# Kernel optimization log

Measured on AMD Instinct MI355X. Metric: run time of the kernel, lower is better.

## Reference

```python
import jax, jax.numpy as jnp
import numpy as np
import math

B, N, C = 32, 576, 1024
INNER, H = 256, 4
HD = INNER // H
ALPHA = 5.0
EPS = 1e-5

def _layer_norm(x, w, b):
    mu = jnp.mean(x, axis=-1, keepdims=True)
    var = jnp.mean((x - mu) ** 2, axis=-1, keepdims=True)
    return (x - mu) * jax.lax.rsqrt(var + EPS) * w + b

def setup_inputs() -> dict:
    key = jax.random.key(0)
    ks = jax.random.split(key, 20)
    def lin(k, out_d, in_d):
        scale = math.sqrt(6.0 / (in_d + out_d))
        return jax.random.uniform(k, (out_d, in_d), jnp.float32, -scale, scale)
    return {
        'query_features': jax.random.normal(ks[0], (B, N, C), jnp.float32),
        'support_features': jax.random.normal(ks[1], (B, N, C), jnp.float32),
        'support_mask_weights': jax.random.uniform(ks[2], (B, N), jnp.float32),
        'ln_q_w': jnp.ones((C,), jnp.float32), 'ln_q_b': jnp.zeros((C,), jnp.float32),
        'ln_s_w': jnp.ones((C,), jnp.float32), 'ln_s_b': jnp.zeros((C,), jnp.float32),
        'Wq': lin(ks[3], INNER, C), 'bq': jnp.zeros((INNER,), jnp.float32),
        'Wk': lin(ks[4], INNER, C), 'bk': jnp.zeros((INNER,), jnp.float32),
        'Wv': lin(ks[5], INNER, C), 'bv': jnp.zeros((INNER,), jnp.float32),
        'Wo': lin(ks[6], C, INNER), 'bo': jnp.zeros((C,), jnp.float32),
        'Wg': 0.02 * jax.random.normal(ks[7], (C, C), jnp.float32),
        'bg': jnp.full((C,), -1.0, jnp.float32),
    }

def reference(query_features, support_features, support_mask_weights,
              ln_q_w, ln_q_b, ln_s_w, ln_s_b,
              Wq, bq, Wk, bk, Wv, bv, Wo, bo, Wg, bg):
    q = _layer_norm(query_features, ln_q_w, ln_q_b)
    s = _layer_norm(support_features, ln_s_w, ln_s_b)
    Q = (q @ Wq.T + bq).reshape(B, N, H, HD).transpose(0, 2, 1, 3)  # (B,H,N,HD)
    K = (s @ Wk.T + bk).reshape(B, N, H, HD).transpose(0, 2, 1, 3)
    V = (s @ Wv.T + bv).reshape(B, N, H, HD).transpose(0, 2, 1, 3)
    logits = jnp.einsum('bhnd,bhmd->bhnm', Q, K) / math.sqrt(HD)
    logits = logits + ALPHA * support_mask_weights[:, None, None, :]
    attn = jax.nn.softmax(logits, axis=-1)
    ctx = jnp.einsum('bhnm,bhmd->bhnd', attn, V).transpose(0, 2, 1, 3).reshape(B, N, INNER)
    out = ctx @ Wo.T + bo
    gate = jax.nn.sigmoid(query_features @ Wg.T + bg)
    enhanced = query_features + gate * out
    return enhanced, attn
```

## Files before the change

kernel.cpp:

```cpp
#include <hip/hip_runtime.h>
#include <hip/hip_bf16.h>
#include <math.h>

#define B_ 32
#define N_ 576
#define C_ 1024
#define INNER_ 256
#define H_ 4
#define HD_ 64
#define M_ (B_*N_)
#define ALPHA_ 5.0f
#define EPS_ 1e-5f

typedef __attribute__((ext_vector_type(8))) short bf16x8;
typedef __attribute__((ext_vector_type(4))) float f32x4;
typedef __attribute__((ext_vector_type(4))) unsigned int u32x4;
typedef unsigned short u16;

__device__ inline u16 bfbits(float x) {
    union { __hip_bfloat16 h; u16 u; } c; c.h = __float2bfloat16(x); return c.u;
}
__device__ inline unsigned pack2bf(float a, float b) {
    return (unsigned)bfbits(a) | ((unsigned)bfbits(b) << 16);
}

template<int WRITE_RAW>
__global__ void ln_fused_kernel(const float* __restrict__ X, const float* __restrict__ w,
                                const float* __restrict__ b, u16* __restrict__ outln,
                                u16* __restrict__ outraw) {
    int row = blockIdx.x * 4 + (threadIdx.x >> 6);
    int lane = threadIdx.x & 63;
    const float* xp = X + (size_t)row * C_;
    float4 v[4];
    #pragma unroll
    for (int j = 0; j < 4; ++j) v[j] = *(const float4*)(xp + lane*4 + j*256);
    float s = 0.f, s2 = 0.f;
    #pragma unroll
    for (int j = 0; j < 4; ++j) {
        s  += v[j].x + v[j].y + v[j].z + v[j].w;
        s2 += v[j].x*v[j].x + v[j].y*v[j].y + v[j].z*v[j].z + v[j].w*v[j].w;
    }
    #pragma unroll
    for (int m = 32; m; m >>= 1) {
        s  += __shfl_xor(s,  m, 64);
        s2 += __shfl_xor(s2, m, 64);
    }
    float mean = s * (1.f/C_);
    float rs = rsqrtf(s2 * (1.f/C_) - mean*mean + EPS_);
    #pragma unroll
    for (int j = 0; j < 4; ++j) {
        int k = lane*4 + j*256;
        float4 wv = *(const float4*)(w + k);
        float4 bv = *(const float4*)(b + k);
        ushort4 o;
        o.x = bfbits((v[j].x - mean)*rs*wv.x + bv.x);
        o.y = bfbits((v[j].y - mean)*rs*wv.y + bv.y);
        o.z = bfbits((v[j].z - mean)*rs*wv.z + bv.z);
        o.w = bfbits((v[j].w - mean)*rs*wv.w + bv.w);
        *(ushort4*)(outln + (size_t)row*C_ + k) = o;
        if (WRITE_RAW) {
            ushort4 r4;
            r4.x = bfbits(v[j].x); r4.y = bfbits(v[j].y);
            r4.z = bfbits(v[j].z); r4.w = bfbits(v[j].w);
            *(ushort4*)(outraw + (size_t)row*C_ + k) = r4;
        }
    }
}

__global__ void cvt_weights_kernel(const float* __restrict__ Wq, const float* __restrict__ Wk,
                                   const float* __restrict__ Wv, const float* __restrict__ Wo,
                                   const float* __restrict__ Wg,
                                   const float* __restrict__ bk, const float* __restrict__ bv,
                                   u16* __restrict__ Wq_b, u16* __restrict__ Wkv_b,
                                   u16* __restrict__ Wo_b, u16* __restrict__ Wg_b,
                                   float* __restrict__ bkv) {
    if (blockIdx.x == 0 && threadIdx.x < 128) {
        float4 t = (threadIdx.x < 64) ? ((const float4*)bk)[threadIdx.x]
                                      : ((const float4*)bv)[threadIdx.x - 64];
        ((float4*)bkv)[threadIdx.x] = t;
    }
    int g = blockIdx.x * 256 + threadIdx.x;
    const float* src; u16* dst; size_t off;
    if (g < 32768)       { src = Wq; dst = Wq_b;          off = (size_t)g*8; }
    else if (g < 65536)  { src = Wk; dst = Wkv_b;         off = (size_t)(g-32768)*8; }
    else if (g < 98304)  { src = Wv; dst = Wkv_b + 262144; off = (size_t)(g-65536)*8; }
    else if (g < 131072) { src = Wo; dst = Wo_b;          off = (size_t)(g-98304)*8; }
    else                 { src = Wg; dst = Wg_b;          off = (size_t)(g-131072)*8; }
    float4 a0 = *(const float4*)(src + off);
    float4 a1 = *(const float4*)(src + off + 4);
    union { u16 s[8]; u32x4 v; } o;
    o.s[0] = bfbits(a0.x); o.s[1] = bfbits(a0.y); o.s[2] = bfbits(a0.z); o.s[3] = bfbits(a0.w);
    o.s[4] = bfbits(a1.x); o.s[5] = bfbits(a1.y); o.s[6] = bfbits(a1.z); o.s[7] = bfbits(a1.w);
    *(u32x4*)(dst + off) = o.v;
}

template<int KDIM, bool F32A>
__device__ inline void gemm_accum(const void* __restrict__ Ap, const u16* __restrict__ Bw,
                                  int row0, int col0, int tid, int lane, int wm, int wn,
                                  u16 (&Asm)[128][72], u16 (&Bsm)[128][72],
                                  f32x4 (&acc)[4][4]) {
    for (int k0 = 0; k0 < KDIM; k0 += 64) {
        #pragma unroll
        for (int i = 0; i < 4; ++i) {
            int s = tid + i*256;
            int r = s >> 3, cg = (s & 7) * 8;
            u32x4 vb = *(const u32x4*)(Bw + (size_t)(col0 + r)*KDIM + k0 + cg);
            if (F32A) {
                const float* a = (const float*)Ap + (size_t)(row0 + r)*KDIM + k0 + cg;
                float4 a0 = *(const float4*)a;
                float4 a1 = *(const float4*)(a + 4);
                union { u16 s[8]; u32x4 v; } o;
                o.s[0]=bfbits(a0.x); o.s[1]=bfbits(a0.y); o.s[2]=bfbits(a0.z); o.s[3]=bfbits(a0.w);
                o.s[4]=bfbits(a1.x); o.s[5]=bfbits(a1.y); o.s[6]=bfbits(a1.z); o.s[7]=bfbits(a1.w);
                *(u32x4*)&Asm[r][cg] = o.v;
            } else {
                *(u32x4*)&Asm[r][cg] =
                    *(const u32x4*)((const u16*)Ap + (size_t)(row0 + r)*KDIM + k0 + cg);
            }
            *(u32x4*)&Bsm[r][cg] = vb;
        }
        __syncthreads();
        #pragma unroll
        for (int ks = 0; ks < 64; ks += 32) {
            bf16x8 af[4], bfr[4];
            #pragma unroll
            for (int i = 0; i < 4; ++i)
                af[i] = *(const bf16x8*)&Asm[wm + i*16 + (lane & 15)][ks + (lane >> 4)*8];
            #pragma unroll
            for (int j = 0; j < 4; ++j)
                bfr[j] = *(const bf16x8*)&Bsm[wn + j*16 + (lane & 15)][ks + (lane >> 4)*8];
            #pragma unroll
            for (int i = 0; i < 4; ++i)
                #pragma unroll
                for (int j = 0; j < 4; ++j)
                    acc[i][j] = __builtin_amdgcn_mfma_f32_16x16x32_bf16(
                        af[i], bfr[j], acc[i][j], 0, 0, 0);
        }
        __syncthreads();
    }
}

template<int NOUT, int KDIM>
__global__ __launch_bounds__(256, 2)
void mfma_gemm_kernel(const u16* __restrict__ A, const u16* __restrict__ Bw,
                      const float* __restrict__ bias, u16* __restrict__ Out) {
    __shared__ u16 Asm[128][72];
    __shared__ u16 Bsm[128][72];
    int tid = threadIdx.x;
    int lane = tid & 63, wid = tid >> 6;
    int wm = (wid >> 1) * 64, wn = (wid & 1) * 64;
    int row0 = blockIdx.y * 128, col0 = blockIdx.x * 128;
    f32x4 acc[4][4] = {};
    gemm_accum<KDIM, false>(A, Bw, row0, col0, tid, lane, wm, wn, Asm, Bsm, acc);
    #pragma unroll
    for (int i = 0; i < 4; ++i) {
        #pragma unroll
        for (int j = 0; j < 4; ++j) {
            int col = col0 + wn + j*16 + (lane & 15);
            float bb = bias[col];
            #pragma unroll
            for (int r = 0; r < 4; ++r) {
                int row = row0 + wm + i*16 + (lane >> 4)*4 + r;
                Out[(size_t)row * NOUT + col] = bfbits(acc[i][j][r] + bb);
            }
        }
    }
}

__global__ __launch_bounds__(256, 2)
void final_fused_kernel(const float* __restrict__ query, const u16* __restrict__ Wg_b,
                        const float* __restrict__ bg,
                        const u16* __restrict__ ctxb, const u16* __restrict__ Wo_b,
                        const float* __restrict__ bo, float* __restrict__ out) {
    __shared__ u16 Asm[128][72];
    __shared__ u16 Bsm[128][72];
    int tid = threadIdx.x;
    int lane = tid & 63, wid = tid >> 6;
    int wm = (wid >> 1) * 64, wn = (wid & 1) * 64;
    int row0 = blockIdx.y * 128, col0 = blockIdx.x * 128;
    f32x4 acc_o[4][4] = {};
    f32x4 acc_g[4][4] = {};
    gemm_accum<INNER_, false>(ctxb, Wo_b, row0, col0, tid, lane, wm, wn, Asm, Bsm, acc_o);
    gemm_accum<C_, true>(query, Wg_b, row0, col0, tid, lane, wm, wn, Asm, Bsm, acc_g);
    #pragma unroll
    for (int i = 0; i < 4; ++i) {
        #pragma unroll
        for (int j = 0; j < 4; ++j) {
            int col = col0 + wn + j*16 + (lane & 15);
            float bgv = bg[col], bov = bo[col];
            #pragma unroll
            for (int r = 0; r < 4; ++r) {
                int row = row0 + wm + i*16 + (lane >> 4)*4 + r;
                size_t idx = (size_t)row * C_ + col;
                float g = 1.f / (1.f + expf(-(acc_g[i][j][r] + bgv)));
                out[idx] = query[idx] + g * (acc_o[i][j][r] + bov);
            }
        }
    }
}

__device__ inline void stage_v_half(const u16* __restrict__ KV, u16* __restrict__ Vt,
                                    int b, int h, int HF, int tid) {
    #pragma unroll
    for (int i = 0; i < 9; ++i) {
        int c = tid + i*256;
        int k = c >> 3;
        int d0 = (c & 7) * 8;
        union { u32x4 v; u16 s[8]; } u;
        u.v = *(const u32x4*)(KV + ((size_t)(b*N_ + HF*288 + k))*512 + 256 + h*HD_ + d0);
        #pragma unroll
        for (int e = 0; e < 8; ++e)
            Vt[(d0 + e)*296 + k] = u.s[e];
    }
}

template<int HF>
__device__ inline void pv_half(const unsigned (&pk)[36][2], f32x4 (&cacc)[4],
                               const u16* __restrict__ Vt, int lane) {
    int s1 = (lane & 15) + ((lane & 16) << 1);
    int s2 = s1 + 16;
    bool hi = (lane & 32) != 0;
    #pragma unroll
    for (int t9 = 0; t9 < 9; ++t9) {
        const int t = HF*9 + t9;
        unsigned A01 = __shfl((int)pk[2*t  ][0], s1, 64);
        unsigned A23 = __shfl((int)pk[2*t  ][1], s1, 64);
        unsigned B01 = __shfl((int)pk[2*t+1][0], s1, 64);
        unsigned B23 = __shfl((int)pk[2*t+1][1], s1, 64);
        unsigned C01 = __shfl((int)pk[2*t  ][0], s2, 64);
        unsigned C23 = __shfl((int)pk[2*t  ][1], s2, 64);
        unsigned D01 = __shfl((int)pk[2*t+1][0], s2, 64);
        unsigned D23 = __shfl((int)pk[2*t+1][1], s2, 64);
        union { unsigned w[4]; bf16x8 v; } bu;
        bu.w[0] = hi ? B01 : A01;
        bu.w[1] = hi ? B23 : A23;
        bu.w[2] = hi ? D01 : C01;
        bu.w[3] = hi ? D23 : C23;
        int colb = 32*t - 288*HF + 8*(lane >> 4);
        #pragma unroll
        for (int dt = 0; dt < 4; ++dt) {
            bf16x8 a = *(const bf16x8*)&Vt[(16*dt + (lane & 15))*296 + colb];
            cacc[dt] = __builtin_amdgcn_mfma_f32_16x16x32_bf16(a, bu.v, cacc[dt], 0, 0, 0);
        }
    }
}

__global__ __launch_bounds__(256, 2)
void attn_mfma_kernel(const u16* __restrict__ Qbf, const u16* __restrict__ KV,
                      const float* __restrict__ mask,
                      float* __restrict__ attn_out, u16* __restrict__ ctxb) {
    __shared__ u16 Vt[64*296];
    __shared__ float Msk[576];
    int tid = threadIdx.x;
    int lane = tid & 63, wid = tid >> 6;
    int bh = blockIdx.y, b = bh >> 2, h = bh & 3;
    int q0 = blockIdx.x * 64;
    int g = lane >> 4;
    int qrow = q0 + wid*16 + (lane & 15);

    if (tid < 144) {
        float4 mv = *(const float4*)(mask + b*N_ + tid*4);
        *(float4*)&Msk[tid*4] = make_float4(ALPHA_*mv.x, ALPHA_*mv.y, ALPHA_*mv.z, ALPHA_*mv.w);
    }
    stage_v_half(KV, Vt, b, h, 0, tid);
    __syncthreads();

    const u16* qp = Qbf + ((size_t)(b*N_) + qrow)*INNER_ + h*HD_ + g*8;
    bf16x8 qf0 = *(const bf16x8*)qp;
    bf16x8 qf1 = *(const bf16x8*)(qp + 32);

    f32x4 acc[36];
    #pragma unroll
    for (int T = 0; T < 36; ++T) acc[T] = (f32x4){0.f, 0.f, 0.f, 0.f};

    const u16* kp = KV + ((size_t)(b*N_) + (lane & 15))*512 + h*HD_ + g*8;
    bf16x8 kb[2][2];
    kb[0][0] = *(const bf16x8*)(kp);
    kb[0][1] = *(const bf16x8*)(kp + 32);
    kb[1][0] = *(const bf16x8*)(kp + 16*512);
    kb[1][1] = *(const bf16x8*)(kp + 16*512 + 32);
    #pragma unroll
    for (int T = 0; T < 36; ++T) {
        bf16x8 n0, n1;
        if (T + 2 < 36) {
            n0 = *(const bf16x8*)(kp + (size_t)(T+2)*16*512);
            n1 = *(const bf16x8*)(kp + (size_t)(T+2)*16*512 + 32);
        }
        acc[T] = __builtin_amdgcn_mfma_f32_16x16x32_bf16(kb[T&1][0], qf0, acc[T], 0, 0, 0);
        acc[T] = __builtin_amdgcn_mfma_f32_16x16x32_bf16(kb[T&1][1], qf1, acc[T], 0, 0, 0);
        if (T + 2 < 36) { kb[T&1][0] = n0; kb[T&1][1] = n1; }
    }

    float m = -1e30f;
    #pragma unroll
    for (int T = 0; T < 36; ++T) {
        float4 mk = *(const float4*)&Msk[16*T + 4*g];
        acc[T][0] = acc[T][0]*0.125f + mk.x;
        acc[T][1] = acc[T][1]*0.125f + mk.y;
        acc[T][2] = acc[T][2]*0.125f + mk.z;
        acc[T][3] = acc[T][3]*0.125f + mk.w;
        m = fmaxf(m, fmaxf(fmaxf(acc[T][0], acc[T][1]), fmaxf(acc[T][2], acc[T][3])));
    }
    m = fmaxf(m, __shfl_xor(m, 16, 64));
    m = fmaxf(m, __shfl_xor(m, 32, 64));

    float l = 0.f;
    #pragma unroll
    for (int T = 0; T < 36; ++T) {
        acc[T][0] = expf(acc[T][0] - m);
        acc[T][1] = expf(acc[T][1] - m);
        acc[T][2] = expf(acc[T][2] - m);
        acc[T][3] = expf(acc[T][3] - m);
        l += acc[T][0] + acc[T][1] + acc[T][2] + acc[T][3];
    }
    l += __shfl_xor(l, 16, 64);
    l += __shfl_xor(l, 32, 64);
    float inv = 1.f / l;

    unsigned pk[36][2];
    float* ap = attn_out + ((size_t)bh*N_ + qrow)*N_;
    #pragma unroll
    for (int T = 0; T < 36; ++T) {
        float e0 = acc[T][0]*inv, e1 = acc[T][1]*inv;
        float e2 = acc[T][2]*inv, e3 = acc[T][3]*inv;
        *(float4*)(ap + 16*T + 4*g) = make_float4(e0, e1, e2, e3);
        pk[T][0] = pack2bf(e0, e1);
        pk[T][1] = pack2bf(e2, e3);
    }

    f32x4 cacc[4] = {};
    pv_half<0>(pk, cacc, Vt, lane);
    __syncthreads();
    stage_v_half(KV, Vt, b, h, 1, tid);
    __syncthreads();
    pv_half<1>(pk, cacc, Vt, lane);

    u16* cp = ctxb + ((size_t)(b*N_) + qrow)*INNER_ + h*HD_ + 4*g;
    #pragma unroll
    for (int dt = 0; dt < 4; ++dt) {
        ushort4 o;
        o.x = bfbits(cacc[dt][0]);
        o.y = bfbits(cacc[dt][1]);
        o.z = bfbits(cacc[dt][2]);
        o.w = bfbits(cacc[dt][3]);
        *(ushort4*)(cp + 16*dt) = o;
    }
}

extern "C" void kernel_launch(void* const* d_in, const int* in_sizes, int n_in,
                              void* d_out, int out_size, void* d_ws, size_t ws_size,
                              hipStream_t stream) {
    const float* query   = (const float*)d_in[0];
    const float* support = (const float*)d_in[1];
    const float* mask    = (const float*)d_in[2];
    const float* ln_q_w  = (const float*)d_in[3];
    const float* ln_q_b  = (const float*)d_in[4];
    const float* ln_s_w  = (const float*)d_in[5];
    const float* ln_s_b  = (const float*)d_in[6];
    const float* Wq      = (const float*)d_in[7];
    const float* bq      = (const float*)d_in[8];
    const float* Wk      = (const float*)d_in[9];
    const float* bk      = (const float*)d_in[10];
    const float* Wv      = (const float*)d_in[11];
    const float* bv      = (const float*)d_in[12];
    const float* Wo      = (const float*)d_in[13];
    const float* bo      = (const float*)d_in[14];
    const float* Wg      = (const float*)d_in[15];
    const float* bg      = (const float*)d_in[16];

    float* out      = (float*)d_out;
    float* attn_out = out + (size_t)M_ * C_;

    char* w = (char*)d_ws;
    u16* Aq    = (u16*)w;  w += (size_t)M_*C_*2;
    u16* As_   = (u16*)w;  w += (size_t)M_*C_*2;
    u16* Wq_b  = (u16*)w;  w += (size_t)INNER_*C_*2;
    u16* Wkv_b = (u16*)w;  w += (size_t)2*INNER_*C_*2;
    u16* Wo_b  = (u16*)w;  w += (size_t)C_*INNER_*2;
    u16* Wg_b  = (u16*)w;  w += (size_t)C_*C_*2;
    float* bkv = (float*)w; w += 512*4;
    u16* Qbf   = (u16*)w;  w += (size_t)M_*INNER_*2;
    u16* KVbf  = (u16*)w;  w += (size_t)M_*2*INNER_*2;
    u16* ctxb  = (u16*)w;  w += (size_t)M_*INNER_*2;

    ln_fused_kernel<0><<<dim3(M_/4), dim3(256), 0, stream>>>(query,   ln_q_w, ln_q_b, Aq,  nullptr);
    ln_fused_kernel<0><<<dim3(M_/4), dim3(256), 0, stream>>>(support, ln_s_w, ln_s_b, As_, nullptr);

    cvt_weights_kernel<<<dim3(1024), dim3(256), 0, stream>>>(
        Wq, Wk, Wv, Wo, Wg, bk, bv, Wq_b, Wkv_b, Wo_b, Wg_b, bkv);

    mfma_gemm_kernel<INNER_, C_><<<dim3(INNER_/128, M_/128), dim3(256), 0, stream>>>(
        Aq, Wq_b, bq, Qbf);
    mfma_gemm_kernel<2*INNER_, C_><<<dim3(2*INNER_/128, M_/128), dim3(256), 0, stream>>>(
        As_, Wkv_b, bkv, KVbf);

    attn_mfma_kernel<<<dim3(N_/64, B_*H_), dim3(256), 0, stream>>>(
        Qbf, KVbf, mask, attn_out, ctxb);

    final_fused_kernel<<<dim3(C_/128, M_/128), dim3(256), 0, stream>>>(
        query, Wg_b, bg, ctxb, Wo_b, bo, out);
}
```

Before: 368.4 us.

## Remap GEMM and attention blocks per XCD and pre-convert query to bf16 in LN

Adds an XCD-aware block index remap so consecutive row tiles run on the same XCD, aiming at better L2 reuse of shared A/B tiles across the GEMMs and the attention kernel. The query LayerNorm kernel now also writes a raw bf16 copy of the query. The final gate GEMM reads that bf16 copy instead of loading fp32 and converting on every tile. The cost is an extra M×C bf16 write in the LN pass and more workspace memory.

```diff
diff --git a/kernel.cpp b/kernel.cpp
--- a/kernel.cpp
+++ b/kernel.cpp
@@ -22,6 +22,15 @@
 }
 __device__ inline unsigned pack2bf(float a, float b) {
     return (unsigned)bfbits(a) | ((unsigned)bfbits(b) << 16);
+}
+
+template<int GX, int GY>
+__device__ inline void xcd_remap(int& col, int& row) {
+    int f = blockIdx.y * GX + blockIdx.x;
+    int xcd = f & 7;
+    int slot = f >> 3;
+    col = slot % GX;
+    row = xcd * (GY >> 3) + slot / GX;
 }
 
 template<int WRITE_RAW>
@@ -94,8 +103,8 @@
     *(u32x4*)(dst + off) = o.v;
 }
 
-template<int KDIM, bool F32A>
-__device__ inline void gemm_accum(const void* __restrict__ Ap, const u16* __restrict__ Bw,
+template<int KDIM>
+__device__ inline void gemm_accum(const u16* __restrict__ Ap, const u16* __restrict__ Bw,
                                   int row0, int col0, int tid, int lane, int wm, int wn,
                                   u16 (&Asm)[128][72], u16 (&Bsm)[128][72],
                                   f32x4 (&acc)[4][4]) {
@@ -104,20 +113,8 @@
         for (int i = 0; i < 4; ++i) {
             int s = tid + i*256;
             int r = s >> 3, cg = (s & 7) * 8;
-            u32x4 vb = *(const u32x4*)(Bw + (size_t)(col0 + r)*KDIM + k0 + cg);
-            if (F32A) {
-                const float* a = (const float*)Ap + (size_t)(row0 + r)*KDIM + k0 + cg;
-                float4 a0 = *(const float4*)a;
-                float4 a1 = *(const float4*)(a + 4);
-                union { u16 s[8]; u32x4 v; } o;
-                o.s[0]=bfbits(a0.x); o.s[1]=bfbits(a0.y); o.s[2]=bfbits(a0.z); o.s[3]=bfbits(a0.w);
-                o.s[4]=bfbits(a1.x); o.s[5]=bfbits(a1.y); o.s[6]=bfbits(a1.z); o.s[7]=bfbits(a1.w);
-                *(u32x4*)&Asm[r][cg] = o.v;
-            } else {
-                *(u32x4*)&Asm[r][cg] =
-                    *(const u32x4*)((const u16*)Ap + (size_t)(row0 + r)*KDIM + k0 + cg);
-            }
-            *(u32x4*)&Bsm[r][cg] = vb;
+            *(u32x4*)&Asm[r][cg] = *(const u32x4*)(Ap + (size_t)(row0 + r)*KDIM + k0 + cg);
+            *(u32x4*)&Bsm[r][cg] = *(const u32x4*)(Bw + (size_t)(col0 + r)*KDIM + k0 + cg);
         }
         __syncthreads();
         #pragma unroll
@@ -140,7 +137,7 @@
     }
 }
 
-template<int NOUT, int KDIM>
+template<int NOUT, int KDIM, int GX, int GY>
 __global__ __launch_bounds__(256, 2)
 void mfma_gemm_kernel(const u16* __restrict__ A, const u16* __restrict__ Bw,
                       const float* __restrict__ bias, u16* __restrict__ Out) {
@@ -149,9 +146,11 @@
     int tid = threadIdx.x;
     int lane = tid & 63, wid = tid >> 6;
     int wm = (wid >> 1) * 64, wn = (wid & 1) * 64;
-    int row0 = blockIdx.y * 128, col0 = blockIdx.x * 128;
+    int bc, br;
+    xcd_remap<GX, GY>(bc, br);
+    int row0 = br * 128, col0 = bc * 128;
     f32x4 acc[4][4] = {};
-    gemm_accum<KDIM, false>(A, Bw, row0, col0, tid, lane, wm, wn, Asm, Bsm, acc);
+    gemm_accum<KDIM>(A, Bw, row0, col0, tid, lane, wm, wn, Asm, Bsm, acc);
     #pragma unroll
     for (int i = 0; i < 4; ++i) {
         #pragma unroll
@@ -168,8 +167,8 @@
 }
 
 __global__ __launch_bounds__(256, 2)
-void final_fused_kernel(const float* __restrict__ query, const u16* __restrict__ Wg_b,
-                        const float* __restrict__ bg,
+void final_fused_kernel(const float* __restrict__ query, const u16* __restrict__ Xq,
+                        const u16* __restrict__ Wg_b, const float* __restrict__ bg,
                         const u16* __restrict__ ctxb, const u16* __restrict__ Wo_b,
                         const float* __restrict__ bo, float* __restrict__ out) {
     __shared__ u16 Asm[128][72];
@@ -177,11 +176,13 @@
     int tid = threadIdx.x;
     int lane = tid & 63, wid = tid >> 6;
     int wm = (wid >> 1) * 64, wn = (wid & 1) * 64;
-    int row0 = blockIdx.y * 128, col0 = blockIdx.x * 128;
+    int bc, br;
+    xcd_remap<8, 144>(bc, br);
+    int row0 = br * 128, col0 = bc * 128;
     f32x4 acc_o[4][4] = {};
     f32x4 acc_g[4][4] = {};
-    gemm_accum<INNER_, false>(ctxb, Wo_b, row0, col0, tid, lane, wm, wn, Asm, Bsm, acc_o);
-    gemm_accum<C_, true>(query, Wg_b, row0, col0, tid, lane, wm, wn, Asm, Bsm, acc_g);
+    gemm_accum<INNER_>(ctxb, Wo_b, row0, col0, tid, lane, wm, wn, Asm, Bsm, acc_o);
+    gemm_accum<C_>(Xq, Wg_b, row0, col0, tid, lane, wm, wn, Asm, Bsm, acc_g);
     #pragma unroll
     for (int i = 0; i < 4; ++i) {
         #pragma unroll
@@ -253,8 +254,10 @@
     __shared__ float Msk[576];
     int tid = threadIdx.x;
     int lane = tid & 63, wid = tid >> 6;
-    int bh = blockIdx.y, b = bh >> 2, h = bh & 3;
-    int q0 = blockIdx.x * 64;
+    int qb, bh;
+    xcd_remap<9, 128>(qb, bh);
+    int b = bh >> 2, h = bh & 3;
+    int q0 = qb * 64;
     int g = lane >> 4;
     int qrow = q0 + wid*16 + (lane & 15);
 
@@ -374,6 +377,7 @@
     char* w = (char*)d_ws;
     u16* Aq    = (u16*)w;  w += (size_t)M_*C_*2;
     u16* As_   = (u16*)w;  w += (size_t)M_*C_*2;
+    u16* Xq    = (u16*)w;  w += (size_t)M_*C_*2;
     u16* Wq_b  = (u16*)w;  w += (size_t)INNER_*C_*2;
     u16* Wkv_b = (u16*)w;  w += (size_t)2*INNER_*C_*2;
     u16* Wo_b  = (u16*)w;  w += (size_t)C_*INNER_*2;
@@ -383,20 +387,20 @@
     u16* KVbf  = (u16*)w;  w += (size_t)M_*2*INNER_*2;
     u16* ctxb  = (u16*)w;  w += (size_t)M_*INNER_*2;
 
-    ln_fused_kernel<0><<<dim3(M_/4), dim3(256), 0, stream>>>(query,   ln_q_w, ln_q_b, Aq,  nullptr);
+    ln_fused_kernel<1><<<dim3(M_/4), dim3(256), 0, stream>>>(query,   ln_q_w, ln_q_b, Aq,  Xq);
     ln_fused_kernel<0><<<dim3(M_/4), dim3(256), 0, stream>>>(support, ln_s_w, ln_s_b, As_, nullptr);
 
     cvt_weights_kernel<<<dim3(1024), dim3(256), 0, stream>>>(
         Wq, Wk, Wv, Wo, Wg, bk, bv, Wq_b, Wkv_b, Wo_b, Wg_b, bkv);
 
-    mfma_gemm_kernel<INNER_, C_><<<dim3(INNER_/128, M_/128), dim3(256), 0, stream>>>(
+    mfma_gemm_kernel<INNER_, C_, 2, 144><<<dim3(2, 144), dim3(256), 0, stream>>>(
         Aq, Wq_b, bq, Qbf);
-    mfma_gemm_kernel<2*INNER_, C_><<<dim3(2*INNER_/128, M_/128), dim3(256), 0, stream>>>(
+    mfma_gemm_kernel<2*INNER_, C_, 4, 144><<<dim3(4, 144), dim3(256), 0, stream>>>(
         As_, Wkv_b, bkv, KVbf);
 
     attn_mfma_kernel<<<dim3(N_/64, B_*H_), dim3(256), 0, stream>>>(
         Qbf, KVbf, mask, attn_out, ctxb);
 
-    final_fused_kernel<<<dim3(C_/128, M_/128), dim3(256), 0, stream>>>(
-        query, Wg_b, bg, ctxb, Wo_b, bo, out);
-}
+    final_fused_kernel<<<dim3(8, 144), dim3(256), 0, stream>>>(
+        query, Xq, Wg_b, bg, ctxb, Wo_b, bo, out);
+}
```

New measurement: 350.9 us. 4.7% less time.

## Merge launches, remap blocks per XCD, use nontemporal stores for outputs

Applied to the files above, without the earlier changes.

Merges the two layer-norm launches into one grid and the Q and KV projection GEMMs into a single launch, which cuts launch overhead and tail effects. Adds an XCD-aware block remap to the GEMM, attention and final kernels so blocks sharing rows of A or the same batch/head land on the same XCD and reuse its L2. Writes the large attention-probability and final outputs with nontemporal stores to avoid polluting cache. The remap assumes the grid splits evenly into 8 XCD groups and that the hardware dispatches blocks round-robin across XCDs.

```diff
diff --git a/kernel.cpp b/kernel.cpp
--- a/kernel.cpp
+++ b/kernel.cpp
@@ -24,10 +24,22 @@
     return (unsigned)bfbits(a) | ((unsigned)bfbits(b) << 16);
 }
 
-template<int WRITE_RAW>
-__global__ void ln_fused_kernel(const float* __restrict__ X, const float* __restrict__ w,
-                                const float* __restrict__ b, u16* __restrict__ outln,
-                                u16* __restrict__ outraw) {
+template<int GX, int GY>
+__device__ inline void xcd_remap(int& col, int& row) {
+    int f = blockIdx.y * GX + blockIdx.x;
+    int xcd = f & 7;
+    int slot = f >> 3;
+    col = slot % GX;
+    row = xcd * (GY >> 3) + slot / GX;
+}
+
+__global__ void ln_fused2_kernel(const float* __restrict__ Xq, const float* __restrict__ Xs,
+                                 const float* __restrict__ wq, const float* __restrict__ bq,
+                                 const float* __restrict__ ws, const float* __restrict__ bs,
+                                 u16* __restrict__ outq, u16* __restrict__ outs) {
+    const float* X; const float* w; const float* b; u16* o;
+    if (blockIdx.y == 0) { X = Xq; w = wq; b = bq; o = outq; }
+    else                 { X = Xs; w = ws; b = bs; o = outs; }
     int row = blockIdx.x * 4 + (threadIdx.x >> 6);
     int lane = threadIdx.x & 63;
     const float* xp = X + (size_t)row * C_;
@@ -52,18 +64,12 @@
         int k = lane*4 + j*256;
         float4 wv = *(const float4*)(w + k);
         float4 bv = *(const float4*)(b + k);
-        ushort4 o;
-        o.x = bfbits((v[j].x - mean)*rs*wv.x + bv.x);
-        o.y = bfbits((v[j].y - mean)*rs*wv.y + bv.y);
-        o.z = bfbits((v[j].z - mean)*rs*wv.z + bv.z);
-        o.w = bfbits((v[j].w - mean)*rs*wv.w + bv.w);
-        *(ushort4*)(outln + (size_t)row*C_ + k) = o;
-        if (WRITE_RAW) {
-            ushort4 r4;
-            r4.x = bfbits(v[j].x); r4.y = bfbits(v[j].y);
-            r4.z = bfbits(v[j].z); r4.w = bfbits(v[j].w);
-            *(ushort4*)(outraw + (size_t)row*C_ + k) = r4;
-        }
+        ushort4 ov;
+        ov.x = bfbits((v[j].x - mean)*rs*wv.x + bv.x);
+        ov.y = bfbits((v[j].y - mean)*rs*wv.y + bv.y);
+        ov.z = bfbits((v[j].z - mean)*rs*wv.z + bv.z);
+        ov.w = bfbits((v[j].w - mean)*rs*wv.w + bv.w);
+        *(ushort4*)(o + (size_t)row*C_ + k) = ov;
     }
 }
 
@@ -140,18 +146,28 @@
     }
 }
 
-template<int NOUT, int KDIM>
 __global__ __launch_bounds__(256, 2)
-void mfma_gemm_kernel(const u16* __restrict__ A, const u16* __restrict__ Bw,
-                      const float* __restrict__ bias, u16* __restrict__ Out) {
+void qkv_gemm_kernel(const u16* __restrict__ Aq, const u16* __restrict__ As,
+                     const u16* __restrict__ Wq_b, const u16* __restrict__ Wkv_b,
+                     const float* __restrict__ bq, const float* __restrict__ bkv,
+                     u16* __restrict__ Qbf, u16* __restrict__ KVbf) {
     __shared__ u16 Asm[128][72];
     __shared__ u16 Bsm[128][72];
     int tid = threadIdx.x;
     int lane = tid & 63, wid = tid >> 6;
     int wm = (wid >> 1) * 64, wn = (wid & 1) * 64;
-    int row0 = blockIdx.y * 128, col0 = blockIdx.x * 128;
+    int bc, br;
+    xcd_remap<6, 144>(bc, br);
+    int row0 = br * 128;
+    bool isQ = (bc < 2);
+    int col0 = (isQ ? bc : bc - 2) * 128;
+    const u16* A  = isQ ? Aq   : As;
+    const u16* Bw = isQ ? Wq_b : Wkv_b;
+    const float* bias = isQ ? bq : bkv;
+    u16* Out = isQ ? Qbf : KVbf;
+    const int NOUT = isQ ? INNER_ : 2*INNER_;
     f32x4 acc[4][4] = {};
-    gemm_accum<KDIM, false>(A, Bw, row0, col0, tid, lane, wm, wn, Asm, Bsm, acc);
+    gemm_accum<C_, false>(A, Bw, row0, col0, tid, lane, wm, wn, Asm, Bsm, acc);
     #pragma unroll
     for (int i = 0; i < 4; ++i) {
         #pragma unroll
@@ -168,8 +184,8 @@
 }
 
 __global__ __launch_bounds__(256, 2)
-void final_fused_kernel(const float* __restrict__ query, const u16* __restrict__ Wg_b,
-                        const float* __restrict__ bg,
+void final_fused_kernel(const float* __restrict__ query,
+                        const u16* __restrict__ Wg_b, const float* __restrict__ bg,
                         const u16* __restrict__ ctxb, const u16* __restrict__ Wo_b,
                         const float* __restrict__ bo, float* __restrict__ out) {
     __shared__ u16 Asm[128][72];
@@ -177,7 +193,9 @@
     int tid = threadIdx.x;
     int lane = tid & 63, wid = tid >> 6;
     int wm = (wid >> 1) * 64, wn = (wid & 1) * 64;
-    int row0 = blockIdx.y * 128, col0 = blockIdx.x * 128;
+    int bc, br;
+    xcd_remap<8, 144>(bc, br);
+    int row0 = br * 128, col0 = bc * 128;
     f32x4 acc_o[4][4] = {};
     f32x4 acc_g[4][4] = {};
     gemm_accum<INNER_, false>(ctxb, Wo_b, row0, col0, tid, lane, wm, wn, Asm, Bsm, acc_o);
@@ -193,7 +211,7 @@
                 int row = row0 + wm + i*16 + (lane >> 4)*4 + r;
                 size_t idx = (size_t)row * C_ + col;
                 float g = 1.f / (1.f + expf(-(acc_g[i][j][r] + bgv)));
-                out[idx] = query[idx] + g * (acc_o[i][j][r] + bov);
+                __builtin_nontemporal_store(query[idx] + g * (acc_o[i][j][r] + bov), &out[idx]);
             }
         }
     }
@@ -253,8 +271,10 @@
     __shared__ float Msk[576];
     int tid = threadIdx.x;
     int lane = tid & 63, wid = tid >> 6;
-    int bh = blockIdx.y, b = bh >> 2, h = bh & 3;
-    int q0 = blockIdx.x * 64;
+    int qb, bh;
+    xcd_remap<9, 128>(qb, bh);
+    int b = bh >> 2, h = bh & 3;
+    int q0 = qb * 64;
     int g = lane >> 4;
     int qrow = q0 + wid*16 + (lane & 15);
 
@@ -323,7 +343,8 @@
     for (int T = 0; T < 36; ++T) {
         float e0 = acc[T][0]*inv, e1 = acc[T][1]*inv;
         float e2 = acc[T][2]*inv, e3 = acc[T][3]*inv;
-        *(float4*)(ap + 16*T + 4*g) = make_float4(e0, e1, e2, e3);
+        f32x4 ov = {e0, e1, e2, e3};
+        __builtin_nontemporal_store(ov, (f32x4*)(ap + 16*T + 4*g));
         pk[T][0] = pack2bf(e0, e1);
         pk[T][1] = pack2bf(e2, e3);
     }
@@ -383,20 +404,18 @@
     u16* KVbf  = (u16*)w;  w += (size_t)M_*2*INNER_*2;
     u16* ctxb  = (u16*)w;  w += (size_t)M_*INNER_*2;
 
-    ln_fused_kernel<0><<<dim3(M_/4), dim3(256), 0, stream>>>(query,   ln_q_w, ln_q_b, Aq,  nullptr);
-    ln_fused_kernel<0><<<dim3(M_/4), dim3(256), 0, stream>>>(support, ln_s_w, ln_s_b, As_, nullptr);
+    ln_fused2_kernel<<<dim3(M_/4, 2), dim3(256), 0, stream>>>(
+        query, support, ln_q_w, ln_q_b, ln_s_w, ln_s_b, Aq, As_);
 
     cvt_weights_kernel<<<dim3(1024), dim3(256), 0, stream>>>(
         Wq, Wk, Wv, Wo, Wg, bk, bv, Wq_b, Wkv_b, Wo_b, Wg_b, bkv);
 
-    mfma_gemm_kernel<INNER_, C_><<<dim3(INNER_/128, M_/128), dim3(256), 0, stream>>>(
-        Aq, Wq_b, bq, Qbf);
-    mfma_gemm_kernel<2*INNER_, C_><<<dim3(2*INNER_/128, M_/128), dim3(256), 0, stream>>>(
-        As_, Wkv_b, bkv, KVbf);
+    qkv_gemm_kernel<<<dim3(6, 144), dim3(256), 0, stream>>>(
+        Aq, As_, Wq_b, Wkv_b, bq, bkv, Qbf, KVbf);
 
     attn_mfma_kernel<<<dim3(N_/64, B_*H_), dim3(256), 0, stream>>>(
         Qbf, KVbf, mask, attn_out, ctxb);
 
-    final_fused_kernel<<<dim3(C_/128, M_/128), dim3(256), 0, stream>>>(
+    final_fused_kernel<<<dim3(8, 144), dim3(256), 0, stream>>>(
         query, Wg_b, bg, ctxb, Wo_b, bo, out);
 }
```

After: 307.9 us. -16.4%, faster.
